# Kernel optimization log

Hardware: AMD Instinct MI355X
Metric: run time of the kernel (lower is better)

## Reference

```python
import jax, jax.numpy as jnp
import numpy as np

SCALE = 8.0  # sqrt(d_head=64)

def setup_inputs() -> dict:
    key = jax.random.key(0)
    kq, kk, kv = jax.random.split(key, 3)
    B, H, S, D = 2, 16, 2048, 64
    q = jax.random.normal(kq, (B, H, S, D), dtype=jnp.float32)
    k = jax.random.normal(kk, (B, H, S, D), dtype=jnp.float32)
    v = jax.random.normal(kv, (B, H, S, D), dtype=jnp.float32)
    return {"q": q, "k": k, "v": v}

def reference(q, k, v):
    # attn = softmax((q/scale) @ k^T, axis=-1); out = attn @ v
    scores = jnp.einsum('bhqd,bhkd->bhqk', q / SCALE, k)  # [B,H,S,S]
    attn = jax.nn.softmax(scores, axis=-1)
    out = jnp.einsum('bhqk,bhkd->bhqd', attn, v)          # [B,H,S,D]
    return (attn, out)
```

## Files before the change

### kernel.cpp

```cpp
#include <hip/hip_runtime.h>


#define S_LEN 2048
#define D_HEAD 64
#define QB 64
#define KB 128
#define NCHUNK (S_LEN / KB)
#define KPAD 72
#define PPAD 136
#define ATTN_ELEMS 134217728ull
#define LOG2E 1.44269504088896340736f

typedef short short8 __attribute__((ext_vector_type(8)));
typedef _Float16 half8 __attribute__((ext_vector_type(8)));
typedef float f32x16 __attribute__((ext_vector_type(16)));
typedef float floatx4 __attribute__((ext_vector_type(4)));
typedef unsigned short ushort8v __attribute__((ext_vector_type(8)));

#if __has_builtin(__builtin_amdgcn_exp2f)
#define EXP2F(x) __builtin_amdgcn_exp2f(x)
#else
#define EXP2F(x) exp2f(x)
#endif

static __device__ __forceinline__ unsigned short f2bf(float f) {
  unsigned u = __builtin_bit_cast(unsigned, f);
  u += 0x7fffu + ((u >> 16) & 1u);
  return (unsigned short)(u >> 16);
}
static __device__ __forceinline__ float bf2f(unsigned short h) {
  unsigned u = ((unsigned)h) << 16;
  return __builtin_bit_cast(float, u);
}
static __device__ __forceinline__ unsigned short f2h(float f) {
  return __builtin_bit_cast(unsigned short, (_Float16)f);
}

__global__ __launch_bounds__(512, 4) void k_rowsum(
    const float* __restrict__ q, const float* __restrict__ k,
    float* __restrict__ outbuf) {
  __shared__ __align__(16) unsigned short KhiS[KB * KPAD];
  __shared__ __align__(16) unsigned short KloS[KB * KPAD];
  __shared__ float rsum_s[QB];

  const int tid = threadIdx.x;
  const int lane = tid & 63;
  const int wid = tid >> 6;
  const int rg = wid & 1, cg = wid >> 1;
  const int bh = blockIdx.x >> 5;
  const int qt = blockIdx.x & 31;

  const float* Q = q + (size_t)bh * S_LEN * D_HEAD;
  const float* K = k + (size_t)bh * S_LEN * D_HEAD;
  float* rinv_out = outbuf + ATTN_ELEMS + (size_t)bh * S_LEN * D_HEAD +
                    (size_t)qt * QB * D_HEAD;

  if (tid < QB) rsum_s[tid] = 0.0f;

  const int arow = qt * QB + rg * 32 + (lane & 31);
  const float* qp = Q + (size_t)arow * D_HEAD + ((lane >> 5) * 8);
  short8 ahi[4], alo[4];
#pragma unroll
  for (int ks = 0; ks < 4; ++ks) {
    floatx4 x0 = *(const floatx4*)(qp + ks * 16);
    floatx4 x1 = *(const floatx4*)(qp + ks * 16 + 4);
    ushort8v uh, ul;
#pragma unroll
    for (int j = 0; j < 4; ++j) {
      float xa = x0[j] * 0.125f;
      unsigned short ha = f2bf(xa);
      uh[j] = ha; ul[j] = f2bf(xa - bf2f(ha));
      float xb = x1[j] * 0.125f;
      unsigned short hb = f2bf(xb);
      uh[4 + j] = hb; ul[4 + j] = f2bf(xb - bf2f(hb));
    }
    ahi[ks] = __builtin_bit_cast(short8, uh);
    alo[ks] = __builtin_bit_cast(short8, ul);
  }

  float psum[16];
#pragma unroll
  for (int i = 0; i < 16; ++i) psum[i] = 0.0f;

  const int srow = tid >> 2;
  const int scol = (tid & 3) * 16;
  const int bcol = cg * 32 + (lane & 31);
  const int boff = (lane >> 5) * 8;

  for (int ch = 0; ch < NCHUNK; ++ch) {
    const int kk0 = ch * KB;
    {
      const float* src = K + (size_t)(kk0 + srow) * D_HEAD + scol;
      floatx4 v0 = *(const floatx4*)(src);
      floatx4 v1 = *(const floatx4*)(src + 4);
      floatx4 v2 = *(const floatx4*)(src + 8);
      floatx4 v3 = *(const floatx4*)(src + 12);
      ushort8v h0, h1, l0, l1;
#pragma unroll
      for (int j = 0; j < 4; ++j) {
        unsigned short a0 = f2bf(v0[j]); h0[j] = a0; l0[j] = f2bf(v0[j] - bf2f(a0));
        unsigned short a1 = f2bf(v1[j]); h0[4+j] = a1; l0[4+j] = f2bf(v1[j] - bf2f(a1));
        unsigned short a2 = f2bf(v2[j]); h1[j] = a2; l1[j] = f2bf(v2[j] - bf2f(a2));
        unsigned short a3 = f2bf(v3[j]); h1[4+j] = a3; l1[4+j] = f2bf(v3[j] - bf2f(a3));
      }
      *(ushort8v*)&KhiS[srow * KPAD + scol] = h0;
      *(ushort8v*)&KhiS[srow * KPAD + scol + 8] = h1;
      *(ushort8v*)&KloS[srow * KPAD + scol] = l0;
      *(ushort8v*)&KloS[srow * KPAD + scol + 8] = l1;
    }
    __syncthreads();
    f32x16 acc = {};
#pragma unroll
    for (int ks = 0; ks < 4; ++ks) {
      ushort8v bhu = *(const ushort8v*)&KhiS[bcol * KPAD + ks * 16 + boff];
      ushort8v blu = *(const ushort8v*)&KloS[bcol * KPAD + ks * 16 + boff];
      short8 bh8 = __builtin_bit_cast(short8, bhu);
      short8 bl8 = __builtin_bit_cast(short8, blu);
      acc = __builtin_amdgcn_mfma_f32_32x32x16_bf16(alo[ks], bh8, acc, 0, 0, 0);
      acc = __builtin_amdgcn_mfma_f32_32x32x16_bf16(ahi[ks], bl8, acc, 0, 0, 0);
      acc = __builtin_amdgcn_mfma_f32_32x32x16_bf16(ahi[ks], bh8, acc, 0, 0, 0);
    }
#pragma unroll
    for (int i = 0; i < 16; ++i) psum[i] += EXP2F(acc[i] * LOG2E);
    __syncthreads();
  }

#pragma unroll
  for (int off = 1; off < 32; off <<= 1) {
#pragma unroll
    for (int i = 0; i < 16; ++i) psum[i] += __shfl_xor(psum[i], off, 64);
  }
  if ((lane & 31) == 0) {
    const int rbase = rg * 32 + 4 * (lane >> 5);
#pragma unroll
    for (int i = 0; i < 16; ++i)
      atomicAdd(&rsum_s[rbase + (i & 3) + 8 * (i >> 2)], psum[i]);
  }
  __syncthreads();
  if (tid < QB) rinv_out[tid] = 1.0f / rsum_s[tid];
}

__global__ __launch_bounds__(512, 4) void k_attn(
    const float* __restrict__ q, const float* __restrict__ k,
    const float* __restrict__ v, float* __restrict__ outbuf) {
  __shared__ __align__(16) unsigned short KhiS[KB * KPAD];
  __shared__ __align__(16) unsigned short KloS[KB * KPAD];
  __shared__ __align__(16) unsigned short Pst[QB * PPAD];
  __shared__ __align__(16) unsigned short VtS[D_HEAD * PPAD];
  __shared__ float rinv_s[QB];

  const int tid = threadIdx.x;
  const int lane = tid & 63;
  const int wid = tid >> 6;
  const int rg = wid & 1, cg = wid >> 1;
  const int dg = (wid >> 1) & 1, kh = wid >> 2;
  const int bh = blockIdx.x >> 5;
  const int qt = blockIdx.x & 31;

  const float* Q = q + (size_t)bh * S_LEN * D_HEAD;
  const float* K = k + (size_t)bh * S_LEN * D_HEAD;
  const float* V = v + (size_t)bh * S_LEN * D_HEAD;
  float* attn_base = outbuf + (size_t)bh * S_LEN * S_LEN + (size_t)qt * QB * S_LEN;
  float* out_base = outbuf + ATTN_ELEMS + (size_t)bh * S_LEN * D_HEAD +
                    (size_t)qt * QB * D_HEAD;

  if (tid < QB) rinv_s[tid] = out_base[tid];

  const int arow = qt * QB + rg * 32 + (lane & 31);
  const float* qp = Q + (size_t)arow * D_HEAD + ((lane >> 5) * 8);
  short8 ahi[4], alo[4];
#pragma unroll
  for (int ks = 0; ks < 4; ++ks) {
    floatx4 x0 = *(const floatx4*)(qp + ks * 16);
    floatx4 x1 = *(const floatx4*)(qp + ks * 16 + 4);
    ushort8v uh, ul;
#pragma unroll
    for (int j = 0; j < 4; ++j) {
      float xa = x0[j] * 0.125f;
      unsigned short ha = f2bf(xa);
      uh[j] = ha; ul[j] = f2bf(xa - bf2f(ha));
      float xb = x1[j] * 0.125f;
      unsigned short hb = f2bf(xb);
      uh[4 + j] = hb; ul[4 + j] = f2bf(xb - bf2f(hb));
    }
    ahi[ks] = __builtin_bit_cast(short8, uh);
    alo[ks] = __builtin_bit_cast(short8, ul);
  }
  __syncthreads();

  floatx4 rvec[4];
  {
    const int rb = rg * 32 + 4 * (lane >> 5);
#pragma unroll
    for (int m = 0; m < 4; ++m) rvec[m] = *(const floatx4*)&rinv_s[rb + 8 * m];
  }

  f32x16 oacc = {};
  const int srow = tid >> 2;
  const int scol = (tid & 3) * 16;
  const int bcol = cg * 32 + (lane & 31);
  const int boff = (lane >> 5) * 8;

  for (int ch = 0; ch < NCHUNK; ++ch) {
    const int kk0 = ch * KB;
    {
      const float* src = K + (size_t)(kk0 + srow) * D_HEAD + scol;
      floatx4 v0 = *(const floatx4*)(src);
      floatx4 v1 = *(const floatx4*)(src + 4);
      floatx4 v2 = *(const floatx4*)(src + 8);
      floatx4 v3 = *(const floatx4*)(src + 12);
      ushort8v h0, h1, l0, l1;
#pragma unroll
      for (int j = 0; j < 4; ++j) {
        unsigned short a0 = f2bf(v0[j]); h0[j] = a0; l0[j] = f2bf(v0[j] - bf2f(a0));
        unsigned short a1 = f2bf(v1[j]); h0[4+j] = a1; l0[4+j] = f2bf(v1[j] - bf2f(a1));
        unsigned short a2 = f2bf(v2[j]); h1[j] = a2; l1[j] = f2bf(v2[j] - bf2f(a2));
        unsigned short a3 = f2bf(v3[j]); h1[4+j] = a3; l1[4+j] = f2bf(v3[j] - bf2f(a3));
      }
      *(ushort8v*)&KhiS[srow * KPAD + scol] = h0;
      *(ushort8v*)&KhiS[srow * KPAD + scol + 8] = h1;
      *(ushort8v*)&KloS[srow * KPAD + scol] = l0;
      *(ushort8v*)&KloS[srow * KPAD + scol + 8] = l1;
    }
    {
#pragma unroll
      for (int half = 0; half < 2; ++half) {
        const float* vsrc = V + (size_t)(kk0 + half * 64 + wid * 8) * D_HEAD + lane;
        ushort8v hv;
#pragma unroll
        for (int i = 0; i < 8; ++i) hv[i] = f2h(vsrc[(size_t)i * D_HEAD]);
        *(ushort8v*)&VtS[lane * PPAD + half * 64 + wid * 8] = hv;
      }
    }
    __syncthreads();

    f32x16 acc = {};
#pragma unroll
    for (int ks = 0; ks < 4; ++ks) {
      ushort8v bhu = *(const ushort8v*)&KhiS[bcol * KPAD + ks * 16 + boff];
      ushort8v blu = *(const ushort8v*)&KloS[bcol * KPAD + ks * 16 + boff];
      short8 bh8 = __builtin_bit_cast(short8, bhu);
      short8 bl8 = __builtin_bit_cast(short8, blu);
      acc = __builtin_amdgcn_mfma_f32_32x32x16_bf16(alo[ks], bh8, acc, 0, 0, 0);
      acc = __builtin_amdgcn_mfma_f32_32x32x16_bf16(ahi[ks], bl8, acc, 0, 0, 0);
      acc = __builtin_amdgcn_mfma_f32_32x32x16_bf16(ahi[ks], bh8, acc, 0, 0, 0);
    }

    {
      const int rbase = rg * 32 + 4 * (lane >> 5);
      const int colg = kk0 + cg * 32 + (lane & 31);
#pragma unroll
      for (int i = 0; i < 16; ++i) {
        float p = EXP2F(acc[i] * LOG2E);
        float at = p * rvec[i >> 2][i & 3];
        const int rl = rbase + (i & 3) + 8 * (i >> 2);
        __builtin_nontemporal_store(at, &attn_base[(size_t)rl * S_LEN + colg]);
        Pst[rl * PPAD + cg * 32 + (lane & 31)] = f2h(at);
      }
    }
    __syncthreads();

#pragma unroll
    for (int ks = 0; ks < 4; ++ks) {
      const int kofs = kh * 64 + ks * 16 + boff;
      ushort8v pu = *(const ushort8v*)&Pst[(rg * 32 + (lane & 31)) * PPAD + kofs];
      ushort8v vu = *(const ushort8v*)&VtS[(dg * 32 + (lane & 31)) * PPAD + kofs];
      oacc = __builtin_amdgcn_mfma_f32_32x32x16_f16(
          __builtin_bit_cast(half8, pu), __builtin_bit_cast(half8, vu), oacc, 0, 0, 0);
    }
    __syncthreads();
  }

  float* red = (float*)KhiS;
  const int t4 = wid & 3;
  if (kh == 1) {
#pragma unroll
    for (int i = 0; i < 16; ++i) red[t4 * 1024 + i * 64 + lane] = oacc[i];
  }
  __syncthreads();
  if (kh == 0) {
#pragma unroll
    for (int i = 0; i < 16; ++i) oacc[i] += red[t4 * 1024 + i * 64 + lane];
    const int rbase = rg * 32 + 4 * (lane >> 5);
#pragma unroll
    for (int i = 0; i < 16; ++i) {
      const int rl = rbase + (i & 3) + 8 * (i >> 2);
      out_base[(size_t)rl * D_HEAD + dg * 32 + (lane & 31)] = oacc[i];
    }
  }
}

extern "C" void kernel_launch(void* const* d_in, const int* in_sizes, int n_in,
                              void* d_out, int out_size, void* d_ws, size_t ws_size,
                              hipStream_t stream) {
  const float* q = (const float*)d_in[0];
  const float* k = (const float*)d_in[1];
  const float* v = (const float*)d_in[2];
  float* out = (float*)d_out;
  (void)d_ws; (void)ws_size; (void)in_sizes; (void)n_in; (void)out_size;

  dim3 grid(32 * (S_LEN / QB));
  dim3 blk(512);
  hipLaunchKernelGGL(k_rowsum, grid, blk, 0, stream, q, k, out);
  hipLaunchKernelGGL(k_attn, grid, blk, 0, stream, q, k, v, out);
}
```

Measured before the change: 783.2 us.

## Precompute split-bf16 K and transposed fp16 V into workspace once

Adds prep kernels that convert K into hi/lo bf16 halves and transpose V into fp16 once per call, storing them in workspace. The rowsum and attention kernels then load MFMA operands straight from global memory, with no per-block conversion, no LDS staging of K and V, and fewer barriers. Blocks are also remapped so consecutive launches spread across heads. This costs two extra launches and extra workspace traffic. A fallback keeps the old path when the workspace is too small.

```diff
diff --git a/kernel.cpp b/kernel.cpp
--- a/kernel.cpp
+++ b/kernel.cpp
@@ -11,6 +11,12 @@
 #define ATTN_ELEMS 134217728ull
 #define LOG2E 1.44269504088896340736f
 
+#define WSE_KHI 0ull
+#define WSE_KLO 4194304ull
+#define WSE_VT  8388608ull
+#define WSE_RINV 12582912ull
+#define WS_NEEDED_BYTES (12582912ull * 2ull + 65536ull * 4ull)
+
 typedef short short8 __attribute__((ext_vector_type(8)));
 typedef _Float16 half8 __attribute__((ext_vector_type(8)));
 typedef float f32x16 __attribute__((ext_vector_type(16)));
@@ -34,6 +40,241 @@
 }
 static __device__ __forceinline__ unsigned short f2h(float f) {
   return __builtin_bit_cast(unsigned short, (_Float16)f);
+}
+
+__global__ __launch_bounds__(512) void k_prep_k(
+    const float* __restrict__ kin, unsigned short* __restrict__ khi,
+    unsigned short* __restrict__ klo) {
+  const size_t base = ((size_t)blockIdx.x * 512 + threadIdx.x) * 8;
+  floatx4 a = *(const floatx4*)(kin + base);
+  floatx4 b = *(const floatx4*)(kin + base + 4);
+  ushort8v h, l;
+#pragma unroll
+  for (int j = 0; j < 4; ++j) {
+    unsigned short ha = f2bf(a[j]); h[j] = ha; l[j] = f2bf(a[j] - bf2f(ha));
+    unsigned short hb = f2bf(b[j]); h[4 + j] = hb; l[4 + j] = f2bf(b[j] - bf2f(hb));
+  }
+  *(ushort8v*)(khi + base) = h;
+  *(ushort8v*)(klo + base) = l;
+}
+
+__global__ __launch_bounds__(512) void k_prep_v(
+    const float* __restrict__ vin, unsigned short* __restrict__ vt) {
+  __shared__ __align__(16) unsigned short T[64 * KPAD];
+  const int tid = threadIdx.x;
+  const int bh = blockIdx.x >> 3;
+  const int part = blockIdx.x & 7;
+  const float* V = vin + (size_t)bh * S_LEN * D_HEAD;
+  unsigned short* Vt = vt + (size_t)bh * D_HEAD * S_LEN;
+
+  const int kk_l = tid >> 3;
+  const int d0 = (tid & 7) * 8;
+  const int dd = tid >> 3;
+  const int kb = (tid & 7) * 8;
+
+  for (int t = part * 4; t < part * 4 + 4; ++t) {
+    const int kk0 = t * 64;
+    floatx4 a = *(const floatx4*)(V + (size_t)(kk0 + kk_l) * D_HEAD + d0);
+    floatx4 b = *(const floatx4*)(V + (size_t)(kk0 + kk_l) * D_HEAD + d0 + 4);
+#pragma unroll
+    for (int j = 0; j < 4; ++j) {
+      T[(d0 + j) * KPAD + kk_l] = f2h(a[j]);
+      T[(d0 + 4 + j) * KPAD + kk_l] = f2h(b[j]);
+    }
+    __syncthreads();
+    *(ushort8v*)(Vt + (size_t)dd * S_LEN + kk0 + kb) = *(const ushort8v*)&T[dd * KPAD + kb];
+    __syncthreads();
+  }
+}
+
+__global__ __launch_bounds__(512, 4) void k_rowsum_f(
+    const float* __restrict__ q, const unsigned short* __restrict__ khi,
+    const unsigned short* __restrict__ klo, float* __restrict__ rinv) {
+  __shared__ float rsum_s[QB];
+  const int tid = threadIdx.x;
+  const int lane = tid & 63;
+  const int wid = tid >> 6;
+  const int rg = wid & 1, cg = wid >> 1;
+  const int bxs = (blockIdx.x & 7) * 128 + (blockIdx.x >> 3);
+  const int bh = bxs >> 5;
+  const int qt = bxs & 31;
+
+  const float* Q = q + (size_t)bh * S_LEN * D_HEAD;
+  const unsigned short* KH = khi + (size_t)bh * S_LEN * D_HEAD;
+  const unsigned short* KL = klo + (size_t)bh * S_LEN * D_HEAD;
+
+  if (tid < QB) rsum_s[tid] = 0.0f;
+
+  const int arow = qt * QB + rg * 32 + (lane & 31);
+  const float* qp = Q + (size_t)arow * D_HEAD + ((lane >> 5) * 8);
+  short8 ahi[4], alo[4];
+#pragma unroll
+  for (int ks = 0; ks < 4; ++ks) {
+    floatx4 x0 = *(const floatx4*)(qp + ks * 16);
+    floatx4 x1 = *(const floatx4*)(qp + ks * 16 + 4);
+    ushort8v uh, ul;
+#pragma unroll
+    for (int j = 0; j < 4; ++j) {
+      float xa = x0[j] * 0.125f; unsigned short ha = f2bf(xa);
+      uh[j] = ha; ul[j] = f2bf(xa - bf2f(ha));
+      float xb = x1[j] * 0.125f; unsigned short hb = f2bf(xb);
+      uh[4 + j] = hb; ul[4 + j] = f2bf(xb - bf2f(hb));
+    }
+    ahi[ks] = __builtin_bit_cast(short8, uh);
+    alo[ks] = __builtin_bit_cast(short8, ul);
+  }
+
+  float psum[16];
+#pragma unroll
+  for (int i = 0; i < 16; ++i) psum[i] = 0.0f;
+
+  const size_t brow0 = (size_t)(cg * 32 + (lane & 31)) * D_HEAD + (lane >> 5) * 8;
+
+  for (int ch = 0; ch < NCHUNK; ++ch) {
+    const size_t cbase = (size_t)ch * KB * D_HEAD + brow0;
+    f32x16 acc = {};
+#pragma unroll
+    for (int ks = 0; ks < 4; ++ks) {
+      ushort8v bhu = *(const ushort8v*)(KH + cbase + ks * 16);
+      ushort8v blu = *(const ushort8v*)(KL + cbase + ks * 16);
+      short8 bh8 = __builtin_bit_cast(short8, bhu);
+      short8 bl8 = __builtin_bit_cast(short8, blu);
+      acc = __builtin_amdgcn_mfma_f32_32x32x16_bf16(alo[ks], bh8, acc, 0, 0, 0);
+      acc = __builtin_amdgcn_mfma_f32_32x32x16_bf16(ahi[ks], bl8, acc, 0, 0, 0);
+      acc = __builtin_amdgcn_mfma_f32_32x32x16_bf16(ahi[ks], bh8, acc, 0, 0, 0);
+    }
+#pragma unroll
+    for (int i = 0; i < 16; ++i) psum[i] += EXP2F(acc[i] * LOG2E);
+  }
+
+#pragma unroll
+  for (int off = 1; off < 32; off <<= 1) {
+#pragma unroll
+    for (int i = 0; i < 16; ++i) psum[i] += __shfl_xor(psum[i], off, 64);
+  }
+  if ((lane & 31) == 0) {
+    const int rbase = rg * 32 + 4 * (lane >> 5);
+#pragma unroll
+    for (int i = 0; i < 16; ++i)
+      atomicAdd(&rsum_s[rbase + (i & 3) + 8 * (i >> 2)], psum[i]);
+  }
+  __syncthreads();
+  if (tid < QB)
+    rinv[(size_t)bh * S_LEN + qt * QB + tid] = 1.0f / rsum_s[tid];
+}
+
+__global__ __launch_bounds__(512, 4) void k_attn_f(
+    const float* __restrict__ q, const unsigned short* __restrict__ khi,
+    const unsigned short* __restrict__ klo, const unsigned short* __restrict__ vt,
+    const float* __restrict__ rinv, float* __restrict__ outbuf) {
+  __shared__ __align__(16) unsigned short Pst[QB * PPAD];
+  __shared__ float rinv_s[QB];
+
+  const int tid = threadIdx.x;
+  const int lane = tid & 63;
+  const int wid = tid >> 6;
+  const int rg = wid & 1, cg = wid >> 1;
+  const int dg = (wid >> 1) & 1, kh = wid >> 2;
+  const int bxs = (blockIdx.x & 7) * 128 + (blockIdx.x >> 3);
+  const int bh = bxs >> 5;
+  const int qt = bxs & 31;
+
+  const float* Q = q + (size_t)bh * S_LEN * D_HEAD;
+  const unsigned short* KH = khi + (size_t)bh * S_LEN * D_HEAD;
+  const unsigned short* KL = klo + (size_t)bh * S_LEN * D_HEAD;
+  const unsigned short* VT = vt + (size_t)bh * D_HEAD * S_LEN;
+  float* attn_base = outbuf + (size_t)bh * S_LEN * S_LEN + (size_t)qt * QB * S_LEN;
+  float* out_base = outbuf + ATTN_ELEMS + (size_t)bh * S_LEN * D_HEAD +
+                    (size_t)qt * QB * D_HEAD;
+
+  if (tid < QB) rinv_s[tid] = rinv[(size_t)bh * S_LEN + qt * QB + tid];
+
+  const int arow = qt * QB + rg * 32 + (lane & 31);
+  const float* qp = Q + (size_t)arow * D_HEAD + ((lane >> 5) * 8);
+  short8 ahi[4], alo[4];
+#pragma unroll
+  for (int ks = 0; ks < 4; ++ks) {
+    floatx4 x0 = *(const floatx4*)(qp + ks * 16);
+    floatx4 x1 = *(const floatx4*)(qp + ks * 16 + 4);
+    ushort8v uh, ul;
+#pragma unroll
+    for (int j = 0; j < 4; ++j) {
+      float xa = x0[j] * 0.125f; unsigned short ha = f2bf(xa);
+      uh[j] = ha; ul[j] = f2bf(xa - bf2f(ha));
+      float xb = x1[j] * 0.125f; unsigned short hb = f2bf(xb);
+      uh[4 + j] = hb; ul[4 + j] = f2bf(xb - bf2f(hb));
+    }
+    ahi[ks] = __builtin_bit_cast(short8, uh);
+    alo[ks] = __builtin_bit_cast(short8, ul);
+  }
+  __syncthreads();
+
+  floatx4 rvec[4];
+  {
+    const int rb = rg * 32 + 4 * (lane >> 5);
+#pragma unroll
+    for (int m = 0; m < 4; ++m) rvec[m] = *(const floatx4*)&rinv_s[rb + 8 * m];
+  }
+
+  f32x16 oacc = {};
+  const size_t brow0 = (size_t)(cg * 32 + (lane & 31)) * D_HEAD + (lane >> 5) * 8;
+  const int boff = (lane >> 5) * 8;
+
+  for (int ch = 0; ch < NCHUNK; ++ch) {
+    const int kk0 = ch * KB;
+    f32x16 acc = {};
+    const size_t cbase = (size_t)kk0 * D_HEAD + brow0;
+#pragma unroll
+    for (int ks = 0; ks < 4; ++ks) {
+      ushort8v bhu = *(const ushort8v*)(KH + cbase + ks * 16);
+      ushort8v blu = *(const ushort8v*)(KL + cbase + ks * 16);
+      short8 bh8 = __builtin_bit_cast(short8, bhu);
+      short8 bl8 = __builtin_bit_cast(short8, blu);
+      acc = __builtin_amdgcn_mfma_f32_32x32x16_bf16(alo[ks], bh8, acc, 0, 0, 0);
+      acc = __builtin_amdgcn_mfma_f32_32x32x16_bf16(ahi[ks], bl8, acc, 0, 0, 0);
+      acc = __builtin_amdgcn_mfma_f32_32x32x16_bf16(ahi[ks], bh8, acc, 0, 0, 0);
+    }
+    {
+      const int rbase = rg * 32 + 4 * (lane >> 5);
+      const int colg = kk0 + cg * 32 + (lane & 31);
+#pragma unroll
+      for (int i = 0; i < 16; ++i) {
+        float p = EXP2F(acc[i] * LOG2E);
+        float at = p * rvec[i >> 2][i & 3];
+        const int rl = rbase + (i & 3) + 8 * (i >> 2);
+        __builtin_nontemporal_store(at, &attn_base[(size_t)rl * S_LEN + colg]);
+        Pst[rl * PPAD + cg * 32 + (lane & 31)] = f2h(at);
+      }
+    }
+    __syncthreads();
+#pragma unroll
+    for (int ks = 0; ks < 4; ++ks) {
+      const int kofs = kh * 64 + ks * 16 + boff;
+      ushort8v pu = *(const ushort8v*)&Pst[(rg * 32 + (lane & 31)) * PPAD + kofs];
+      ushort8v vu = *(const ushort8v*)(VT + (size_t)(dg * 32 + (lane & 31)) * S_LEN + kk0 + kofs);
+      oacc = __builtin_amdgcn_mfma_f32_32x32x16_f16(
+          __builtin_bit_cast(half8, pu), __builtin_bit_cast(half8, vu), oacc, 0, 0, 0);
+    }
+    __syncthreads();
+  }
+
+  float* red = (float*)Pst;
+  const int t4 = wid & 3;
+  if (kh == 1) {
+#pragma unroll
+    for (int i = 0; i < 16; ++i) red[t4 * 1024 + i * 64 + lane] = oacc[i];
+  }
+  __syncthreads();
+  if (kh == 0) {
+#pragma unroll
+    for (int i = 0; i < 16; ++i) oacc[i] += red[t4 * 1024 + i * 64 + lane];
+    const int rbase = rg * 32 + 4 * (lane >> 5);
+#pragma unroll
+    for (int i = 0; i < 16; ++i) {
+      const int rl = rbase + (i & 3) + 8 * (i >> 2);
+      out_base[(size_t)rl * D_HEAD + dg * 32 + (lane & 31)] = oacc[i];
+    }
+  }
 }
 
 __global__ __launch_bounds__(512, 4) void k_rowsum(
@@ -42,21 +283,17 @@
   __shared__ __align__(16) unsigned short KhiS[KB * KPAD];
   __shared__ __align__(16) unsigned short KloS[KB * KPAD];
   __shared__ float rsum_s[QB];
-
   const int tid = threadIdx.x;
   const int lane = tid & 63;
   const int wid = tid >> 6;
   const int rg = wid & 1, cg = wid >> 1;
   const int bh = blockIdx.x >> 5;
   const int qt = blockIdx.x & 31;
-
   const float* Q = q + (size_t)bh * S_LEN * D_HEAD;
   const float* K = k + (size_t)bh * S_LEN * D_HEAD;
   float* rinv_out = outbuf + ATTN_ELEMS + (size_t)bh * S_LEN * D_HEAD +
                     (size_t)qt * QB * D_HEAD;
-
   if (tid < QB) rsum_s[tid] = 0.0f;
-
   const int arow = qt * QB + rg * 32 + (lane & 31);
   const float* qp = Q + (size_t)arow * D_HEAD + ((lane >> 5) * 8);
   short8 ahi[4], alo[4];
@@ -67,26 +304,21 @@
     ushort8v uh, ul;
 #pragma unroll
     for (int j = 0; j < 4; ++j) {
-      float xa = x0[j] * 0.125f;
-      unsigned short ha = f2bf(xa);
+      float xa = x0[j] * 0.125f; unsigned short ha = f2bf(xa);
       uh[j] = ha; ul[j] = f2bf(xa - bf2f(ha));
-      float xb = x1[j] * 0.125f;
-      unsigned short hb = f2bf(xb);
+      float xb = x1[j] * 0.125f; unsigned short hb = f2bf(xb);
       uh[4 + j] = hb; ul[4 + j] = f2bf(xb - bf2f(hb));
     }
     ahi[ks] = __builtin_bit_cast(short8, uh);
     alo[ks] = __builtin_bit_cast(short8, ul);
   }
-
   float psum[16];
 #pragma unroll
   for (int i = 0; i < 16; ++i) psum[i] = 0.0f;
-
   const int srow = tid >> 2;
   const int scol = (tid & 3) * 16;
   const int bcol = cg * 32 + (lane & 31);
   const int boff = (lane >> 5) * 8;
-
   for (int ch = 0; ch < NCHUNK; ++ch) {
     const int kk0 = ch * KB;
     {
@@ -124,7 +356,6 @@
     for (int i = 0; i < 16; ++i) psum[i] += EXP2F(acc[i] * LOG2E);
     __syncthreads();
   }
-
 #pragma unroll
   for (int off = 1; off < 32; off <<= 1) {
 #pragma unroll
@@ -148,7 +379,6 @@
   __shared__ __align__(16) unsigned short Pst[QB * PPAD];
   __shared__ __align__(16) unsigned short VtS[D_HEAD * PPAD];
   __shared__ float rinv_s[QB];
-
   const int tid = threadIdx.x;
   const int lane = tid & 63;
   const int wid = tid >> 6;
@@ -156,16 +386,13 @@
   const int dg = (wid >> 1) & 1, kh = wid >> 2;
   const int bh = blockIdx.x >> 5;
   const int qt = blockIdx.x & 31;
-
   const float* Q = q + (size_t)bh * S_LEN * D_HEAD;
   const float* K = k + (size_t)bh * S_LEN * D_HEAD;
   const float* V = v + (size_t)bh * S_LEN * D_HEAD;
   float* attn_base = outbuf + (size_t)bh * S_LEN * S_LEN + (size_t)qt * QB * S_LEN;
   float* out_base = outbuf + ATTN_ELEMS + (size_t)bh * S_LEN * D_HEAD +
                     (size_t)qt * QB * D_HEAD;
-
   if (tid < QB) rinv_s[tid] = out_base[tid];
-
   const int arow = qt * QB + rg * 32 + (lane & 31);
   const float* qp = Q + (size_t)arow * D_HEAD + ((lane >> 5) * 8);
   short8 ahi[4], alo[4];
@@ -176,31 +403,26 @@
     ushort8v uh, ul;
 #pragma unroll
     for (int j = 0; j < 4; ++j) {
-      float xa = x0[j] * 0.125f;
-      unsigned short ha = f2bf(xa);
+      float xa = x0[j] * 0.125f; unsigned short ha = f2bf(xa);
       uh[j] = ha; ul[j] = f2bf(xa - bf2f(ha));
-      float xb = x1[j] * 0.125f;
-      unsigned short hb = f2bf(xb);
+      float xb = x1[j] * 0.125f; unsigned short hb = f2bf(xb);
       uh[4 + j] = hb; ul[4 + j] = f2bf(xb - bf2f(hb));
     }
     ahi[ks] = __builtin_bit_cast(short8, uh);
     alo[ks] = __builtin_bit_cast(short8, ul);
   }
   __syncthreads();
-
   floatx4 rvec[4];
   {
     const int rb = rg * 32 + 4 * (lane >> 5);
 #pragma unroll
     for (int m = 0; m < 4; ++m) rvec[m] = *(const floatx4*)&rinv_s[rb + 8 * m];
   }
-
   f32x16 oacc = {};
   const int srow = tid >> 2;
   const int scol = (tid & 3) * 16;
   const int bcol = cg * 32 + (lane & 31);
   const int boff = (lane >> 5) * 8;
-
   for (int ch = 0; ch < NCHUNK; ++ch) {
     const int kk0 = ch * KB;
     {
@@ -233,7 +455,6 @@
       }
     }
     __syncthreads();
-
     f32x16 acc = {};
 #pragma unroll
     for (int ks = 0; ks < 4; ++ks) {
@@ -245,7 +466,6 @@
       acc = __builtin_amdgcn_mfma_f32_32x32x16_bf16(ahi[ks], bl8, acc, 0, 0, 0);
       acc = __builtin_amdgcn_mfma_f32_32x32x16_bf16(ahi[ks], bh8, acc, 0, 0, 0);
     }
-
     {
       const int rbase = rg * 32 + 4 * (lane >> 5);
       const int colg = kk0 + cg * 32 + (lane & 31);
@@ -259,7 +479,6 @@
       }
     }
     __syncthreads();
-
 #pragma unroll
     for (int ks = 0; ks < 4; ++ks) {
       const int kofs = kh * 64 + ks * 16 + boff;
@@ -270,7 +489,6 @@
     }
     __syncthreads();
   }
-
   float* red = (float*)KhiS;
   const int t4 = wid & 3;
   if (kh == 1) {
@@ -297,10 +515,21 @@
   const float* k = (const float*)d_in[1];
   const float* v = (const float*)d_in[2];
   float* out = (float*)d_out;
-  (void)d_ws; (void)ws_size; (void)in_sizes; (void)n_in; (void)out_size;
-
-  dim3 grid(32 * (S_LEN / QB));
+  (void)in_sizes; (void)n_in; (void)out_size;
+
   dim3 blk(512);
-  hipLaunchKernelGGL(k_rowsum, grid, blk, 0, stream, q, k, out);
-  hipLaunchKernelGGL(k_attn, grid, blk, 0, stream, q, k, v, out);
-}
+  if (ws_size >= WS_NEEDED_BYTES) {
+    unsigned short* wsu = (unsigned short*)d_ws;
+    unsigned short* khi = wsu + WSE_KHI;
+    unsigned short* klo = wsu + WSE_KLO;
+    unsigned short* vt = wsu + WSE_VT;
+    float* rinv = (float*)(wsu + WSE_RINV);
+    hipLaunchKernelGGL(k_prep_k, dim3(1024), blk, 0, stream, k, khi, klo);
+    hipLaunchKernelGGL(k_prep_v, dim3(256), blk, 0, stream, v, vt);
+    hipLaunchKernelGGL(k_rowsum_f, dim3(1024), blk, 0, stream, q, khi, klo, rinv);
+    hipLaunchKernelGGL(k_attn_f, dim3(1024), blk, 0, stream, q, khi, klo, vt, rinv, out);
+  } else {
+    hipLaunchKernelGGL(k_rowsum, dim3(1024), blk, 0, stream, q, k, out);
+    hipLaunchKernelGGL(k_attn, dim3(1024), blk, 0, stream, q, k, v, out);
+  }
+}
```

Result: slower. 829.0 us (+5.8%).
